# Performance work log

Hardware: AMD Instinct MI355X
Metric: run time of the kernel (lower is better)

The kernel has to match this reference:

```python
import jax, jax.numpy as jnp
import numpy as np
from jax import lax

BETA = 0.9   # membrane decay
THR = 1.0    # firing threshold (soft reset)
K = 10       # number of time bins
# spatial pyramid for original_shape=(100,368) under 4 stride-2 SAME convs
HW = [(50, 184), (25, 92), (13, 46), (7, 23)]
CH = [4, 8, 16, 32]


def conv(x, w, b, stride=1):
    y = lax.conv_general_dilated(x, w, (stride, stride), 'SAME',
                                 dimension_numbers=('NCHW', 'OIHW', 'NCHW'))
    return y + b[None, :, None, None]


def spike(u):
    # heaviside forward, sigmoid straight-through surrogate backward
    s = (u > 0.0).astype(u.dtype)
    sg = jax.nn.sigmoid(4.0 * u)
    return sg + lax.stop_gradient(s - sg)


def setup_inputs() -> dict:
    key = jax.random.key(0)
    ks = jax.random.split(key, 12)
    T, B = 1000, 1
    x = jax.random.normal(ks[0], (T, B, 1, 100, 368), jnp.float32)

    def w(k, o, i, kh=3, kw=3):
        return 0.1 * jax.random.normal(k, (o, i, kh, kw), jnp.float32)

    inp = {'x': x}
    cin = [1] + CH[:3]
    for li in range(4):
        inp['w%d' % (li + 1)] = w(ks[1 + li], CH[li], cin[li])
        inp['b%d' % (li + 1)] = jnp.zeros((CH[li],), jnp.float32)
    sc = [2 * K * c for c in CH]  # skip channels: [80,160,320,640]
    inp['dw4'] = w(ks[5], 64, sc[3]); inp['db4'] = jnp.zeros((64,), jnp.float32)
    inp['dw3'] = w(ks[6], 32, 64 + sc[2]); inp['db3'] = jnp.zeros((32,), jnp.float32)
    inp['dw2'] = w(ks[7], 16, 32 + sc[1]); inp['db2'] = jnp.zeros((16,), jnp.float32)
    inp['dw1'] = w(ks[8], 8, 16 + sc[0]); inp['db1'] = jnp.zeros((8,), jnp.float32)
    inp['wo'] = w(ks[9], 1, 8, 1, 1); inp['bo'] = jnp.zeros((1,), jnp.float32)
    inp['total_steps'] = 1000
    inp['block_size'] = 100
    return inp


def reference(x, w1, b1, w2, b2, w3, b3, w4, b4,
              dw4, db4, dw3, db3, dw2, db2, dw1, db1, wo, bo,
              total_steps, block_size):
    S = total_steps // K  # steps per bin
    B = x.shape[1]
    xb = x.reshape((K, S) + x.shape[1:])  # [K,S,B,C,H,W]
    mems0 = tuple(jnp.zeros((B, CH[i], HW[i][0], HW[i][1]), x.dtype) for i in range(4))
    enc_w = [(w1, b1), (w2, b2), (w3, b3), (w4, b4)]

    def forward_step(x_t, mems):
        new_mems, spk = [], x_t
        for (wi, bi), m in zip(enc_w, mems):
            m = BETA * m + conv(spk, wi, bi, 2)
            spk = spike(m - THR)
            m = m - spk * THR  # soft reset
            new_mems.append(m)
        return tuple(new_mems)

    def step(carry, x_t):
        mems, sums, sqs = carry
        mems = forward_step(x_t, mems)
        sums = tuple(s + m for s, m in zip(sums, mems))
        sqs = tuple(q + m * m for q, m in zip(sqs, mems))
        return (mems, sums, sqs), None

    def bin_fn(mems, x_bin):
        zeros = tuple(jnp.zeros_like(m) for m in mems)
        (mems, sums, sqs), _ = lax.scan(step, (mems, zeros, zeros), x_bin)
        means = tuple(s / S for s in sums)
        stds = tuple(jnp.sqrt(jnp.maximum(q / S - mu * mu, 1e-8))
                     for q, mu in zip(sqs, means))
        return mems, (means, stds)

    _, (means, stds) = lax.scan(bin_fn, mems0, xb)  # each leaf: [K,B,C,H,W]

    def skip(mean, std):
        # torch.cat([mean0,std0,mean1,std1,...], dim=1) channel ordering
        f = jnp.stack([mean, std], axis=1)        # [K,2,B,C,H,W]
        f = jnp.transpose(f, (2, 0, 1, 3, 4, 5))  # [B,K,2,C,H,W]
        b_, k_, t_, c_, h_, w_ = f.shape
        return f.reshape(b_, k_ * t_ * c_, h_, w_)

    skips = [skip(means[i], stds[i]) for i in range(4)]

    def up(t, hw):
        return jax.image.resize(t, (t.shape[0], t.shape[1], hw[0], hw[1]), 'bilinear')

    relu = jax.nn.relu
    d = relu(conv(skips[3], dw4, db4))
    d = relu(conv(jnp.concatenate([up(d, HW[2]), skips[2]], 1), dw3, db3))
    d = relu(conv(jnp.concatenate([up(d, HW[1]), skips[1]], 1), dw2, db2))
    d = relu(conv(jnp.concatenate([up(d, HW[0]), skips[0]], 1), dw1, db1))
    tau_c = conv(up(d, (100, 368)), wo, bo)  # [B,1,100,368]
    return tau_c
```

## Files before the change

kernel.cpp:

```cpp
#include <hip/hip_runtime.h>

#define KBINS  10
#define SBIN   100
#define BETA   0.9f
#define THR    1.0f
#define CDIV(a,b) (((a)+(b)-1)/(b))


__global__ void k_zero16(float4* __restrict__ p, int n16) {
    int i = blockIdx.x * blockDim.x + threadIdx.x;
    if (i < n16) p[i] = make_float4(0.f, 0.f, 0.f, 0.f);
}

__global__ void k_conv1(const float* __restrict__ x,
                        const float* __restrict__ w1,
                        const float* __restrict__ b1,
                        float* __restrict__ c1, int tcount) {
    int n = blockIdx.x * blockDim.x + threadIdx.x;
    if (n >= tcount * 50 * 46) return;
    int wq  = n % 46;
    int tmp = n / 46;
    int h   = tmp % 50;
    int t   = tmp / 50;
    int w0  = wq * 4;

    const float* xt = x + (size_t)t * 36800;
    float rm2 = (h  < 49)  ? 1.f : 0.f;
    float cm8 = (w0 < 180) ? 1.f : 0.f;
    int   r2  = min(2 * h + 2, 99);
    int   cb  = 2 * w0;
    int   c8  = min(cb + 8, 367);

    const float* row0 = xt + (2 * h) * 368 + cb;
    const float* row1 = row0 + 368;
    const float* row2 = xt + r2 * 368 + cb;

    float tap[3][9];
    #pragma unroll
    for (int j = 0; j < 8; j++) {
        tap[0][j] = row0[j];
        tap[1][j] = row1[j];
        tap[2][j] = row2[j] * rm2;
    }
    tap[0][8] = xt[(2 * h) * 368 + c8] * cm8;
    tap[1][8] = xt[(2 * h + 1) * 368 + c8] * cm8;
    tap[2][8] = xt[r2 * 368 + c8] * (rm2 * cm8);

    float* ot = c1 + (size_t)t * 36800 + h * 184 + w0;
    #pragma unroll
    for (int co = 0; co < 4; co++) {
        float b = b1[co];
        float a0 = b, a1 = b, a2 = b, a3 = b;
        #pragma unroll
        for (int r = 0; r < 3; r++) {
            #pragma unroll
            for (int kw = 0; kw < 3; kw++) {
                float wv = w1[co * 9 + r * 3 + kw];
                a0 = fmaf(tap[r][0 + kw], wv, a0);
                a1 = fmaf(tap[r][2 + kw], wv, a1);
                a2 = fmaf(tap[r][4 + kw], wv, a2);
                a3 = fmaf(tap[r][6 + kw], wv, a3);
            }
        }
        *(float4*)(ot + (size_t)co * 9200) = make_float4(a0, a1, a2, a3);
    }
}

__global__ void k_scan(const float* __restrict__ cbuf,
                       unsigned char* __restrict__ spk,
                       float* __restrict__ skip,
                       float* __restrict__ mstate,
                       int C, int HW, int Win, int Wp, int HpWp,
                       int write_spk, int bin0, int nbins, int init) {
    const int PF = 10;
    int CHW = C * HW;
    int p = blockIdx.x * blockDim.x + threadIdx.x;
    if (p >= CHW) return;
    int c  = p / HW;
    int hw = p - c * HW;
    int h  = hw / Win, w = hw - h * Win;

    const size_t tstr = (size_t)C * HpWp;
    unsigned char* sp = spk + (size_t)bin0 * SBIN * tstr
                      + (size_t)c * HpWp + (h + 1) * Wp + (w + 1);

    float m = init ? 0.0f : mstate[p];
    float va[PF], vb[PF];
    #pragma unroll
    for (int j = 0; j < PF; j++) va[j] = cbuf[(size_t)j * CHW + p];

    int T = nbins * SBIN;
    for (int k = 0; k < nbins; k++) {
        float s = 0.0f, q = 0.0f;
        for (int b = 0; b < SBIN / PF; b++) {
            int lt0 = k * SBIN + b * PF;
            int ltn = lt0 + PF;
            bool more = (ltn < T);
            #pragma unroll
            for (int j = 0; j < PF; j++)
                vb[j] = more ? cbuf[(size_t)(ltn + j) * CHW + p] : 0.0f;
            #pragma unroll
            for (int j = 0; j < PF; j++) {
                m = fmaf(m, BETA, va[j]);
                float spv = (m - THR > 0.0f) ? 1.0f : 0.0f;
                m -= spv * THR;
                if (write_spk) sp[(size_t)(lt0 + j) * tstr] = (unsigned char)spv;
                s += m;
                q = fmaf(m, m, q);
            }
            #pragma unroll
            for (int j = 0; j < PF; j++) va[j] = vb[j];
        }
        int g = bin0 + k;
        float mean = s * (1.0f / SBIN);
        float var  = q * (1.0f / SBIN) - mean * mean;
        float sd   = sqrtf(fmaxf(var, 1e-8f));
        skip[(size_t)(g * 2 * C + c) * HW + hw]     = mean;
        skip[(size_t)(g * 2 * C + C + c) * HW + hw] = sd;
    }
    mstate[p] = m;
}

template<int CIN, int COUT, int COG, int OW,
         int HOUT, int WOUT, int PADH, int HP, int WP>
__global__ void k_convs2(const unsigned char* __restrict__ spk,
                         const float* __restrict__ wt,
                         const float* __restrict__ bias,
                         float* __restrict__ out, int t0, int tcount) {
    const int WQ = (WOUT + OW - 1) / OW;
    const int NT = 2 * OW + 1;
    int n = blockIdx.x * blockDim.x + threadIdx.x;
    if (n >= tcount * HOUT * WQ) return;
    int wq  = n % WQ;
    int tmp = n / WQ;
    int h   = tmp % HOUT;
    int tl  = tmp / HOUT;
    int cog = blockIdx.y;
    int w0  = wq * OW;

    const unsigned char* base = spk + (size_t)(t0 + tl) * CIN * HP * WP
                              + (2 * h - PADH + 1) * WP + (2 * w0 + 1);

    float acc[OW][COG];
    #pragma unroll
    for (int q = 0; q < OW; q++)
        #pragma unroll
        for (int co = 0; co < COG; co++) acc[q][co] = bias[cog * COG + co];

    for (int ci = 0; ci < CIN; ci++) {
        const unsigned char* ic = base + (size_t)ci * HP * WP;
        float tap[3][NT];
        #pragma unroll
        for (int r = 0; r < 3; r++)
            #pragma unroll
            for (int j = 0; j < NT; j++)
                tap[r][j] = (float)ic[r * WP + j];
        #pragma unroll
        for (int co = 0; co < COG; co++) {
            const float* wc = wt + ((size_t)(cog * COG + co) * CIN + ci) * 9;
            #pragma unroll
            for (int r = 0; r < 3; r++)
                #pragma unroll
                for (int kw = 0; kw < 3; kw++) {
                    float wv = wc[r * 3 + kw];
                    #pragma unroll
                    for (int q = 0; q < OW; q++)
                        acc[q][co] = fmaf(tap[r][2 * q + kw], wv, acc[q][co]);
                }
        }
    }

    float* ot = out + ((size_t)tl * COUT + cog * COG) * (HOUT * WOUT) + h * WOUT + w0;
    #pragma unroll
    for (int co = 0; co < COG; co++) {
        float* oc = ot + (size_t)co * (HOUT * WOUT);
        if constexpr (OW == 4) {
            *(float4*)oc = make_float4(acc[0][co], acc[1][co], acc[2][co], acc[3][co]);
        } else {
            if (w0 + 2 <= WOUT) *(float2*)oc = make_float2(acc[0][co], acc[1][co]);
            else                oc[0] = acc[0][co];
        }
    }
}

__global__ void k_conv_part(const float* __restrict__ in, int Cin, int H, int W,
                            const float* __restrict__ wt,
                            float* __restrict__ part,
                            int Cout, int CS) {
    int HW  = H * W;
    int pix = blockIdx.x * blockDim.x + threadIdx.x;
    if (pix >= HW) return;
    int co    = blockIdx.y;
    int chunk = blockIdx.z;
    int h = pix / W, w = pix - h * W;

    int off[9]; float msk[9];
    #pragma unroll
    for (int kh = 0; kh < 3; kh++) {
        int r = h + kh - 1;
        bool rok = (r >= 0) && (r < H);
        int rc = rok ? r : 0;
        #pragma unroll
        for (int kw = 0; kw < 3; kw++) {
            int cc = w + kw - 1;
            bool cok = (cc >= 0) && (cc < W);
            int ccc = cok ? cc : 0;
            off[kh * 3 + kw] = rc * W + ccc;
            msk[kh * 3 + kw] = (rok && cok) ? 1.0f : 0.0f;
        }
    }

    const float* ibase = in + (size_t)chunk * CS * HW;
    const float* wbase = wt + ((size_t)co * Cin + (size_t)chunk * CS) * 9;
    float acc0 = 0.0f, acc1 = 0.0f;
    for (int ci = 0; ci < CS; ci += 2) {
        const float* ic0 = ibase + (size_t)ci * HW;
        const float* wc0 = wbase + ci * 9;
        #pragma unroll
        for (int j = 0; j < 9; j++)
            acc0 = fmaf(msk[j] * ic0[off[j]], wc0[j], acc0);
        const float* ic1 = ic0 + HW;
        const float* wc1 = wc0 + 9;
        #pragma unroll
        for (int j = 0; j < 9; j++)
            acc1 = fmaf(msk[j] * ic1[off[j]], wc1[j], acc1);
    }
    part[((size_t)chunk * Cout + co) * HW + pix] = acc0 + acc1;
}

__global__ void k_dconv_part(const float* __restrict__ skp, int Cskip,
                             const float* __restrict__ dprev, int Cup,
                             int Hi, int Wi,
                             const float* __restrict__ wt,
                             float* __restrict__ part,
                             int Cout, int CS, int H, int W) {
    int HW  = H * W;
    int pix = blockIdx.x * blockDim.x + threadIdx.x;
    if (pix >= HW) return;
    int co    = blockIdx.y;
    int chunk = blockIdx.z;
    int h = pix / W, w = pix - h * W;
    int Cin = Cup + Cskip;

    int roff[3], h0c[3], h1c[3];
    float rmsk[3], ah[3];
    #pragma unroll
    for (int kh = 0; kh < 3; kh++) {
        int r = h + kh - 1;
        bool rok = (r >= 0) && (r < H);
        roff[kh] = rok ? r : 0;
        rmsk[kh] = rok ? 1.0f : 0.0f;
        float ph = (r + 0.5f) * (float)Hi / (float)H - 0.5f;
        float fh = floorf(ph);
        ah[kh] = ph - fh;
        int hh = (int)fh;
        h0c[kh] = min(max(hh, 0), Hi - 1);
        h1c[kh] = min(max(hh + 1, 0), Hi - 1);
    }
    int coff[3], w0c[3], w1c[3];
    float cmsk[3], aw[3];
    #pragma unroll
    for (int kw = 0; kw < 3; kw++) {
        int cc = w + kw - 1;
        bool cok = (cc >= 0) && (cc < W);
        coff[kw] = cok ? cc : 0;
        cmsk[kw] = cok ? 1.0f : 0.0f;
        float pw = (cc + 0.5f) * (float)Wi / (float)W - 0.5f;
        float fw = floorf(pw);
        aw[kw] = pw - fw;
        int ww = (int)fw;
        w0c[kw] = min(max(ww, 0), Wi - 1);
        w1c[kw] = min(max(ww + 1, 0), Wi - 1);
    }

    float acc0 = 0.0f, acc1 = 0.0f;
    for (int cl = 0; cl < CS; cl++) {
        int ci = chunk * CS + cl;
        const float* wc = wt + ((size_t)co * Cin + ci) * 9;
        float a = 0.0f;
        if (ci < Cup) {
            const float* dc = dprev + (size_t)ci * Hi * Wi;
            #pragma unroll
            for (int kh = 0; kh < 3; kh++) {
                #pragma unroll
                for (int kw = 0; kw < 3; kw++) {
                    float v00 = dc[h0c[kh] * Wi + w0c[kw]];
                    float v01 = dc[h0c[kh] * Wi + w1c[kw]];
                    float v10 = dc[h1c[kh] * Wi + w0c[kw]];
                    float v11 = dc[h1c[kh] * Wi + w1c[kw]];
                    float v = (1.0f - ah[kh]) * ((1.0f - aw[kw]) * v00 + aw[kw] * v01)
                            + ah[kh] * ((1.0f - aw[kw]) * v10 + aw[kw] * v11);
                    a = fmaf(v * rmsk[kh] * cmsk[kw], wc[kh * 3 + kw], a);
                }
            }
        } else {
            const float* ic = skp + (size_t)(ci - Cup) * HW;
            #pragma unroll
            for (int kh = 0; kh < 3; kh++)
                #pragma unroll
                for (int kw = 0; kw < 3; kw++)
                    a = fmaf(rmsk[kh] * cmsk[kw] * ic[roff[kh] * W + coff[kw]],
                             wc[kh * 3 + kw], a);
        }
        if (cl & 1) acc1 += a; else acc0 += a;
    }
    part[((size_t)chunk * Cout + co) * HW + pix] = acc0 + acc1;
}

__global__ void k_reduce_relu(const float* __restrict__ part,
                              const float* __restrict__ bias,
                              float* __restrict__ out,
                              int Cout, int HW, int nchunks) {
    int n = blockIdx.x * blockDim.x + threadIdx.x;
    if (n >= Cout * HW) return;
    int co = n / HW;
    float acc = bias[co];
    for (int c = 0; c < nchunks; c++)
        acc += part[(size_t)c * Cout * HW + n];
    out[n] = fmaxf(acc, 0.0f);
}

__global__ void k_final(const float* __restrict__ d1,
                        const float* __restrict__ wo,
                        const float* __restrict__ bo,
                        float* __restrict__ out) {
    int n = blockIdx.x * blockDim.x + threadIdx.x;
    if (n >= 36800) return;
    int w = n % 368, h = n / 368;
    float ph = (h + 0.5f) * 0.5f - 0.5f;
    float pw = (w + 0.5f) * 0.5f - 0.5f;
    float fh = floorf(ph), fw = floorf(pw);
    int h0 = (int)fh, w0 = (int)fw;
    float ah = ph - fh, aw = pw - fw;
    int h0c = min(max(h0, 0), 49),  h1c = min(max(h0 + 1, 0), 49);
    int w0c = min(max(w0, 0), 183), w1c = min(max(w0 + 1, 0), 183);
    float acc = bo[0];
    #pragma unroll
    for (int c = 0; c < 8; c++) {
        const float* sc = d1 + c * 9200;
        float v00 = sc[h0c * 184 + w0c], v01 = sc[h0c * 184 + w1c];
        float v10 = sc[h1c * 184 + w0c], v11 = sc[h1c * 184 + w1c];
        float v = (1.0f - ah) * ((1.0f - aw) * v00 + aw * v01)
                + ah * ((1.0f - aw) * v10 + aw * v11);
        acc = fmaf(wo[c], v, acc);
    }
    out[n] = acc;
}

extern "C" void kernel_launch(void* const* d_in, const int* in_sizes, int n_in,
                              void* d_out, int out_size, void* d_ws, size_t ws_size,
                              hipStream_t stream) {
    (void)in_sizes; (void)n_in; (void)out_size; (void)ws_size;
    const float* x   = (const float*)d_in[0];
    const float* w1  = (const float*)d_in[1];
    const float* b1  = (const float*)d_in[2];
    const float* w2  = (const float*)d_in[3];
    const float* b2  = (const float*)d_in[4];
    const float* w3  = (const float*)d_in[5];
    const float* b3  = (const float*)d_in[6];
    const float* w4  = (const float*)d_in[7];
    const float* b4  = (const float*)d_in[8];
    const float* dw4 = (const float*)d_in[9];
    const float* db4 = (const float*)d_in[10];
    const float* dw3 = (const float*)d_in[11];
    const float* db3 = (const float*)d_in[12];
    const float* dw2 = (const float*)d_in[13];
    const float* db2 = (const float*)d_in[14];
    const float* dw1 = (const float*)d_in[15];
    const float* db1 = (const float*)d_in[16];
    const float* wo  = (const float*)d_in[17];
    const float* bo  = (const float*)d_in[18];
    float* out = (float*)d_out;

    char* ws = (char*)d_ws;
    size_t off = 0;
    auto alloc = [&](size_t bytes) -> void* {
        void* p = ws + off;
        off += (bytes + 255) & ~(size_t)255;
        return p;
    };
    float*         cbuf  = (float*)alloc(38272000);
    unsigned char* spk1p = (unsigned char*)alloc(39936000);
    unsigned char* spk2p = (unsigned char*)alloc(21600000);
    unsigned char* spk3p = (unsigned char*)alloc(12960000);
    float*         skip0 = (float*)alloc(2944000);
    float*         skip1 = (float*)alloc(1472000);
    float*         skip2 = (float*)alloc(765440);
    float*         skip3 = (float*)alloc(412160);
    float*         ms1   = (float*)alloc(147200);
    float*         ms2   = (float*)alloc(73600);
    char* dec = (char*)cbuf;
    size_t doff = 0;
    auto dalloc = [&](size_t bytes) -> void* {
        void* p = dec + doff;
        doff += (bytes + 255) & ~(size_t)255;
        return p;
    };
    float* d4   = (float*)dalloc(10304u * 4);
    float* d3   = (float*)dalloc(19136u * 4);
    float* d2   = (float*)dalloc(36800u * 4);
    float* d1   = (float*)dalloc(73600u * 4);
    float* part = (float*)dalloc(2500000u);

    const int BS  = 256;
    const int SBS = 64;

    {
        int n16 = (39936000 + 21600000 + 12960000) / 16;
        k_zero16<<<CDIV(n16, BS), BS, 0, stream>>>((float4*)spk1p, n16);
    }

    for (int q = 0; q < 5; q++) {
        k_conv1<<<CDIV(200 * 50 * 46, BS), BS, 0, stream>>>(
            x + (size_t)q * 200 * 36800, w1, b1, cbuf, 200);
        k_scan<<<CDIV(36800, SBS), SBS, 0, stream>>>(
            cbuf, spk1p, skip0, ms1, 4, 9200, 184, 192, 52 * 192,
            1, 2 * q, 2, (q == 0) ? 1 : 0);
    }

    for (int q = 0; q < 2; q++) {
        k_convs2<4, 8, 8, 4, 25, 92, 0, 52, 192>
            <<<dim3(CDIV(500 * 25 * 23, BS), 1), BS, 0, stream>>>(
                spk1p, w2, b2, cbuf, q * 500, 500);
        k_scan<<<CDIV(18400, SBS), SBS, 0, stream>>>(
            cbuf, spk2p, skip1, ms2, 8, 2300, 92, 100, 27 * 100,
            1, 5 * q, 5, (q == 0) ? 1 : 0);
    }

    k_convs2<8, 16, 16, 2, 13, 46, 1, 27, 100>
        <<<dim3(CDIV(1000 * 13 * 23, BS), 1), BS, 0, stream>>>(
            spk2p, w3, b3, cbuf, 0, 1000);
    k_scan<<<CDIV(9568, SBS), SBS, 0, stream>>>(
        cbuf, spk3p, skip2, ms2, 16, 598, 46, 54, 15 * 54, 1, 0, 10, 1);

    k_convs2<16, 32, 16, 2, 7, 23, 1, 15, 54>
        <<<dim3(CDIV(1000 * 7 * 12, BS), 2), BS, 0, stream>>>(
            spk3p, w4, b4, cbuf, 0, 1000);
    k_scan<<<CDIV(5152, SBS), SBS, 0, stream>>>(
        cbuf, spk3p , skip3, ms1 , 32, 161, 23, 31, 9 * 31,
        0, 0, 10, 1);

    {
        dim3 g(CDIV(161, 64), 64, 10);
        k_conv_part<<<g, 64, 0, stream>>>(skip3, 640, 7, 23, dw4, part, 64, 64);
        k_reduce_relu<<<CDIV(64 * 161, BS), BS, 0, stream>>>(part, db4, d4, 64, 161, 10);
    }
    {
        dim3 g(CDIV(598, 64), 32, 8);
        k_dconv_part<<<g, 64, 0, stream>>>(skip2, 320, d4, 64, 7, 23,
                                           dw3, part, 32, 48, 13, 46);
        k_reduce_relu<<<CDIV(32 * 598, BS), BS, 0, stream>>>(part, db3, d3, 32, 598, 8);
    }
    {
        dim3 g(CDIV(2300, BS), 16, 4);
        k_dconv_part<<<g, BS, 0, stream>>>(skip1, 160, d3, 32, 13, 46,
                                           dw2, part, 16, 48, 25, 92);
        k_reduce_relu<<<CDIV(16 * 2300, BS), BS, 0, stream>>>(part, db2, d2, 16, 2300, 4);
    }
    {
        dim3 g(CDIV(9200, BS), 8, 2);
        k_dconv_part<<<g, BS, 0, stream>>>(skip0, 80, d2, 16, 25, 92,
                                           dw1, part, 8, 48, 50, 184);
        k_reduce_relu<<<CDIV(8 * 9200, BS), BS, 0, stream>>>(part, db1, d1, 8, 9200, 2);
    }
    k_final<<<CDIV(36800, BS), BS, 0, stream>>>(d1, wo, bo, out);
}
```

Measured before the change: 968.2 us.

## Run encoder layers over all timesteps at once and fuse decoder reduction via atomics

The time-chunked loops for layers 1 and 2 are replaced by single full-length conv and scan launches, using a much larger conv buffer that holds all 1000 timesteps. This removes the per-chunk membrane state carry and several launches. The decoder's partial-sum buffers and separate reduce+ReLU kernels are replaced by atomicAdd into zeroed outputs, with ReLU moved into the consumers' loads. The scan prefetch depth is raised to 20. In exchange, working-set memory and cache pressure grow, and the atomics make the decoder sums order-dependent.

```diff
diff --git a/kernel.cpp b/kernel.cpp
--- a/kernel.cpp
+++ b/kernel.cpp
@@ -15,9 +15,9 @@
 __global__ void k_conv1(const float* __restrict__ x,
                         const float* __restrict__ w1,
                         const float* __restrict__ b1,
-                        float* __restrict__ c1, int tcount) {
+                        float* __restrict__ c1) {
     int n = blockIdx.x * blockDim.x + threadIdx.x;
-    if (n >= tcount * 50 * 46) return;
+    if (n >= 1000 * 50 * 46) return;
     int wq  = n % 46;
     int tmp = n / 46;
     int h   = tmp % 50;
@@ -69,10 +69,9 @@
 __global__ void k_scan(const float* __restrict__ cbuf,
                        unsigned char* __restrict__ spk,
                        float* __restrict__ skip,
-                       float* __restrict__ mstate,
-                       int C, int HW, int Win, int Wp, int HpWp,
-                       int write_spk, int bin0, int nbins, int init) {
-    const int PF = 10;
+                       float* __restrict__ mscratch,
+                       int C, int HW, int Win, int Wp, int HpWp, int write_spk) {
+    const int PF = 20;
     int CHW = C * HW;
     int p = blockIdx.x * blockDim.x + threadIdx.x;
     if (p >= CHW) return;
@@ -81,44 +80,42 @@
     int h  = hw / Win, w = hw - h * Win;
 
     const size_t tstr = (size_t)C * HpWp;
-    unsigned char* sp = spk + (size_t)bin0 * SBIN * tstr
-                      + (size_t)c * HpWp + (h + 1) * Wp + (w + 1);
-
-    float m = init ? 0.0f : mstate[p];
+    unsigned char* sp = spk + (size_t)c * HpWp + (h + 1) * Wp + (w + 1);
+
+    float m = 0.0f;
     float va[PF], vb[PF];
     #pragma unroll
     for (int j = 0; j < PF; j++) va[j] = cbuf[(size_t)j * CHW + p];
 
-    int T = nbins * SBIN;
-    for (int k = 0; k < nbins; k++) {
+    const int T = KBINS * SBIN;
+    for (int k = 0; k < KBINS; k++) {
         float s = 0.0f, q = 0.0f;
         for (int b = 0; b < SBIN / PF; b++) {
-            int lt0 = k * SBIN + b * PF;
-            int ltn = lt0 + PF;
-            bool more = (ltn < T);
+            int t0 = k * SBIN + b * PF;
+            int tn = t0 + PF;
+            bool more = (tn < T);
             #pragma unroll
             for (int j = 0; j < PF; j++)
-                vb[j] = more ? cbuf[(size_t)(ltn + j) * CHW + p] : 0.0f;
+                vb[j] = more ? cbuf[(size_t)(tn + j) * CHW + p] : 0.0f;
             #pragma unroll
             for (int j = 0; j < PF; j++) {
                 m = fmaf(m, BETA, va[j]);
                 float spv = (m - THR > 0.0f) ? 1.0f : 0.0f;
                 m -= spv * THR;
-                if (write_spk) sp[(size_t)(lt0 + j) * tstr] = (unsigned char)spv;
+                if (write_spk) sp[(size_t)(t0 + j) * tstr] = (unsigned char)spv;
                 s += m;
                 q = fmaf(m, m, q);
             }
             #pragma unroll
             for (int j = 0; j < PF; j++) va[j] = vb[j];
         }
-        int g = bin0 + k;
         float mean = s * (1.0f / SBIN);
         float var  = q * (1.0f / SBIN) - mean * mean;
         float sd   = sqrtf(fmaxf(var, 1e-8f));
-        skip[(size_t)(g * 2 * C + c) * HW + hw]     = mean;
-        skip[(size_t)(g * 2 * C + C + c) * HW + hw] = sd;
-    }
-    mstate[p] = m;
+        skip[(size_t)(k * 2 * C + c) * HW + hw]     = mean;
+        skip[(size_t)(k * 2 * C + C + c) * HW + hw] = sd;
+    }
+    mscratch[p] = m;
 }
 
 template<int CIN, int COUT, int COG, int OW,
@@ -126,19 +123,19 @@
 __global__ void k_convs2(const unsigned char* __restrict__ spk,
                          const float* __restrict__ wt,
                          const float* __restrict__ bias,
-                         float* __restrict__ out, int t0, int tcount) {
+                         float* __restrict__ out) {
     const int WQ = (WOUT + OW - 1) / OW;
     const int NT = 2 * OW + 1;
     int n = blockIdx.x * blockDim.x + threadIdx.x;
-    if (n >= tcount * HOUT * WQ) return;
+    if (n >= 1000 * HOUT * WQ) return;
     int wq  = n % WQ;
     int tmp = n / WQ;
     int h   = tmp % HOUT;
-    int tl  = tmp / HOUT;
+    int t   = tmp / HOUT;
     int cog = blockIdx.y;
     int w0  = wq * OW;
 
-    const unsigned char* base = spk + (size_t)(t0 + tl) * CIN * HP * WP
+    const unsigned char* base = spk + (size_t)t * CIN * HP * WP
                               + (2 * h - PADH + 1) * WP + (2 * w0 + 1);
 
     float acc[OW][COG];
@@ -170,7 +167,7 @@
         }
     }
 
-    float* ot = out + ((size_t)tl * COUT + cog * COG) * (HOUT * WOUT) + h * WOUT + w0;
+    float* ot = out + ((size_t)t * COUT + cog * COG) * (HOUT * WOUT) + h * WOUT + w0;
     #pragma unroll
     for (int co = 0; co < COG; co++) {
         float* oc = ot + (size_t)co * (HOUT * WOUT);
@@ -183,9 +180,10 @@
     }
 }
 
-__global__ void k_conv_part(const float* __restrict__ in, int Cin, int H, int W,
+__global__ void k_dec_conv0(const float* __restrict__ in, int Cin, int H, int W,
                             const float* __restrict__ wt,
-                            float* __restrict__ part,
+                            const float* __restrict__ bias,
+                            float* __restrict__ dout,
                             int Cout, int CS) {
     int HW  = H * W;
     int pix = blockIdx.x * blockDim.x + threadIdx.x;
@@ -212,7 +210,8 @@
 
     const float* ibase = in + (size_t)chunk * CS * HW;
     const float* wbase = wt + ((size_t)co * Cin + (size_t)chunk * CS) * 9;
-    float acc0 = 0.0f, acc1 = 0.0f;
+    float acc0 = (chunk == 0) ? bias[co] : 0.0f;
+    float acc1 = 0.0f;
     for (int ci = 0; ci < CS; ci += 2) {
         const float* ic0 = ibase + (size_t)ci * HW;
         const float* wc0 = wbase + ci * 9;
@@ -225,15 +224,16 @@
         for (int j = 0; j < 9; j++)
             acc1 = fmaf(msk[j] * ic1[off[j]], wc1[j], acc1);
     }
-    part[((size_t)chunk * Cout + co) * HW + pix] = acc0 + acc1;
-}
-
-__global__ void k_dconv_part(const float* __restrict__ skp, int Cskip,
-                             const float* __restrict__ dprev, int Cup,
-                             int Hi, int Wi,
-                             const float* __restrict__ wt,
-                             float* __restrict__ part,
-                             int Cout, int CS, int H, int W) {
+    atomicAdd(&dout[(size_t)co * HW + pix], acc0 + acc1);
+}
+
+__global__ void k_dec_conv(const float* __restrict__ skp, int Cskip,
+                           const float* __restrict__ dprev, int Cup,
+                           int Hi, int Wi,
+                           const float* __restrict__ wt,
+                           const float* __restrict__ bias,
+                           float* __restrict__ dout,
+                           int Cout, int CS, int H, int W) {
     int HW  = H * W;
     int pix = blockIdx.x * blockDim.x + threadIdx.x;
     if (pix >= HW) return;
@@ -273,7 +273,8 @@
         w1c[kw] = min(max(ww + 1, 0), Wi - 1);
     }
 
-    float acc0 = 0.0f, acc1 = 0.0f;
+    float acc0 = (chunk == 0) ? bias[co] : 0.0f;
+    float acc1 = 0.0f;
     for (int cl = 0; cl < CS; cl++) {
         int ci = chunk * CS + cl;
         const float* wc = wt + ((size_t)co * Cin + ci) * 9;
@@ -284,10 +285,10 @@
             for (int kh = 0; kh < 3; kh++) {
                 #pragma unroll
                 for (int kw = 0; kw < 3; kw++) {
-                    float v00 = dc[h0c[kh] * Wi + w0c[kw]];
-                    float v01 = dc[h0c[kh] * Wi + w1c[kw]];
-                    float v10 = dc[h1c[kh] * Wi + w0c[kw]];
-                    float v11 = dc[h1c[kh] * Wi + w1c[kw]];
+                    float v00 = fmaxf(dc[h0c[kh] * Wi + w0c[kw]], 0.0f);
+                    float v01 = fmaxf(dc[h0c[kh] * Wi + w1c[kw]], 0.0f);
+                    float v10 = fmaxf(dc[h1c[kh] * Wi + w0c[kw]], 0.0f);
+                    float v11 = fmaxf(dc[h1c[kh] * Wi + w1c[kw]], 0.0f);
                     float v = (1.0f - ah[kh]) * ((1.0f - aw[kw]) * v00 + aw[kw] * v01)
                             + ah[kh] * ((1.0f - aw[kw]) * v10 + aw[kw] * v11);
                     a = fmaf(v * rmsk[kh] * cmsk[kw], wc[kh * 3 + kw], a);
@@ -304,20 +305,7 @@
         }
         if (cl & 1) acc1 += a; else acc0 += a;
     }
-    part[((size_t)chunk * Cout + co) * HW + pix] = acc0 + acc1;
-}
-
-__global__ void k_reduce_relu(const float* __restrict__ part,
-                              const float* __restrict__ bias,
-                              float* __restrict__ out,
-                              int Cout, int HW, int nchunks) {
-    int n = blockIdx.x * blockDim.x + threadIdx.x;
-    if (n >= Cout * HW) return;
-    int co = n / HW;
-    float acc = bias[co];
-    for (int c = 0; c < nchunks; c++)
-        acc += part[(size_t)c * Cout * HW + n];
-    out[n] = fmaxf(acc, 0.0f);
+    atomicAdd(&dout[(size_t)co * HW + pix], acc0 + acc1);
 }
 
 __global__ void k_final(const float* __restrict__ d1,
@@ -338,8 +326,10 @@
     #pragma unroll
     for (int c = 0; c < 8; c++) {
         const float* sc = d1 + c * 9200;
-        float v00 = sc[h0c * 184 + w0c], v01 = sc[h0c * 184 + w1c];
-        float v10 = sc[h1c * 184 + w0c], v11 = sc[h1c * 184 + w1c];
+        float v00 = fmaxf(sc[h0c * 184 + w0c], 0.0f);
+        float v01 = fmaxf(sc[h0c * 184 + w1c], 0.0f);
+        float v10 = fmaxf(sc[h1c * 184 + w0c], 0.0f);
+        float v11 = fmaxf(sc[h1c * 184 + w1c], 0.0f);
         float v = (1.0f - ah) * ((1.0f - aw) * v00 + aw * v01)
                 + ah * ((1.0f - aw) * v10 + aw * v11);
         acc = fmaf(wo[c], v, acc);
@@ -379,89 +369,67 @@
         off += (bytes + 255) & ~(size_t)255;
         return p;
     };
-    float*         cbuf  = (float*)alloc(38272000);
+    float*         cbuf  = (float*)alloc(147200000);
     unsigned char* spk1p = (unsigned char*)alloc(39936000);
     unsigned char* spk2p = (unsigned char*)alloc(21600000);
     unsigned char* spk3p = (unsigned char*)alloc(12960000);
+    float*         d4    = (float*)alloc(41216);
+    float*         d3    = (float*)alloc(76544);
+    float*         d2    = (float*)alloc(147200);
+    float*         d1    = (float*)alloc(294400);
     float*         skip0 = (float*)alloc(2944000);
     float*         skip1 = (float*)alloc(1472000);
     float*         skip2 = (float*)alloc(765440);
     float*         skip3 = (float*)alloc(412160);
-    float*         ms1   = (float*)alloc(147200);
-    float*         ms2   = (float*)alloc(73600);
-    char* dec = (char*)cbuf;
-    size_t doff = 0;
-    auto dalloc = [&](size_t bytes) -> void* {
-        void* p = dec + doff;
-        doff += (bytes + 255) & ~(size_t)255;
-        return p;
-    };
-    float* d4   = (float*)dalloc(10304u * 4);
-    float* d3   = (float*)dalloc(19136u * 4);
-    float* d2   = (float*)dalloc(36800u * 4);
-    float* d1   = (float*)dalloc(73600u * 4);
-    float* part = (float*)dalloc(2500000u);
+    float*         msS   = (float*)alloc(147200);
 
     const int BS  = 256;
     const int SBS = 64;
 
     {
-        int n16 = (39936000 + 21600000 + 12960000) / 16;
+        size_t nb = 39936000ull + 21600000 + 12960000
+                  + 41216 + 76544 + 147200 + 294400;
+        int n16 = (int)(nb / 16);
         k_zero16<<<CDIV(n16, BS), BS, 0, stream>>>((float4*)spk1p, n16);
     }
 
-    for (int q = 0; q < 5; q++) {
-        k_conv1<<<CDIV(200 * 50 * 46, BS), BS, 0, stream>>>(
-            x + (size_t)q * 200 * 36800, w1, b1, cbuf, 200);
-        k_scan<<<CDIV(36800, SBS), SBS, 0, stream>>>(
-            cbuf, spk1p, skip0, ms1, 4, 9200, 184, 192, 52 * 192,
-            1, 2 * q, 2, (q == 0) ? 1 : 0);
-    }
-
-    for (int q = 0; q < 2; q++) {
-        k_convs2<4, 8, 8, 4, 25, 92, 0, 52, 192>
-            <<<dim3(CDIV(500 * 25 * 23, BS), 1), BS, 0, stream>>>(
-                spk1p, w2, b2, cbuf, q * 500, 500);
-        k_scan<<<CDIV(18400, SBS), SBS, 0, stream>>>(
-            cbuf, spk2p, skip1, ms2, 8, 2300, 92, 100, 27 * 100,
-            1, 5 * q, 5, (q == 0) ? 1 : 0);
-    }
+    k_conv1<<<CDIV(1000 * 50 * 46, BS), BS, 0, stream>>>(x, w1, b1, cbuf);
+    k_scan<<<CDIV(36800, SBS), SBS, 0, stream>>>(cbuf, spk1p, skip0, msS,
+                                                 4, 9200, 184, 192, 52 * 192, 1);
+
+    k_convs2<4, 8, 8, 4, 25, 92, 0, 52, 192>
+        <<<dim3(CDIV(1000 * 25 * 23, BS), 1), BS, 0, stream>>>(spk1p, w2, b2, cbuf);
+    k_scan<<<CDIV(18400, SBS), SBS, 0, stream>>>(cbuf, spk2p, skip1, msS,
+                                                 8, 2300, 92, 100, 27 * 100, 1);
 
     k_convs2<8, 16, 16, 2, 13, 46, 1, 27, 100>
-        <<<dim3(CDIV(1000 * 13 * 23, BS), 1), BS, 0, stream>>>(
-            spk2p, w3, b3, cbuf, 0, 1000);
-    k_scan<<<CDIV(9568, SBS), SBS, 0, stream>>>(
-        cbuf, spk3p, skip2, ms2, 16, 598, 46, 54, 15 * 54, 1, 0, 10, 1);
+        <<<dim3(CDIV(1000 * 13 * 23, BS), 1), BS, 0, stream>>>(spk2p, w3, b3, cbuf);
+    k_scan<<<CDIV(9568, SBS), SBS, 0, stream>>>(cbuf, spk3p, skip2, msS,
+                                                16, 598, 46, 54, 15 * 54, 1);
 
     k_convs2<16, 32, 16, 2, 7, 23, 1, 15, 54>
-        <<<dim3(CDIV(1000 * 7 * 12, BS), 2), BS, 0, stream>>>(
-            spk3p, w4, b4, cbuf, 0, 1000);
-    k_scan<<<CDIV(5152, SBS), SBS, 0, stream>>>(
-        cbuf, spk3p , skip3, ms1 , 32, 161, 23, 31, 9 * 31,
-        0, 0, 10, 1);
+        <<<dim3(CDIV(1000 * 7 * 12, BS), 2), BS, 0, stream>>>(spk3p, w4, b4, cbuf);
+    k_scan<<<CDIV(5152, SBS), SBS, 0, stream>>>(cbuf, spk1p , skip3, msS,
+                                                32, 161, 23, 31, 9 * 31, 0);
 
     {
         dim3 g(CDIV(161, 64), 64, 10);
-        k_conv_part<<<g, 64, 0, stream>>>(skip3, 640, 7, 23, dw4, part, 64, 64);
-        k_reduce_relu<<<CDIV(64 * 161, BS), BS, 0, stream>>>(part, db4, d4, 64, 161, 10);
+        k_dec_conv0<<<g, 64, 0, stream>>>(skip3, 640, 7, 23, dw4, db4, d4, 64, 64);
     }
     {
         dim3 g(CDIV(598, 64), 32, 8);
-        k_dconv_part<<<g, 64, 0, stream>>>(skip2, 320, d4, 64, 7, 23,
-                                           dw3, part, 32, 48, 13, 46);
-        k_reduce_relu<<<CDIV(32 * 598, BS), BS, 0, stream>>>(part, db3, d3, 32, 598, 8);
+        k_dec_conv<<<g, 64, 0, stream>>>(skip2, 320, d4, 64, 7, 23,
+                                         dw3, db3, d3, 32, 48, 13, 46);
     }
     {
-        dim3 g(CDIV(2300, BS), 16, 4);
-        k_dconv_part<<<g, BS, 0, stream>>>(skip1, 160, d3, 32, 13, 46,
-                                           dw2, part, 16, 48, 25, 92);
-        k_reduce_relu<<<CDIV(16 * 2300, BS), BS, 0, stream>>>(part, db2, d2, 16, 2300, 4);
+        dim3 g(CDIV(2300, 128), 16, 4);
+        k_dec_conv<<<g, 128, 0, stream>>>(skip1, 160, d3, 32, 13, 46,
+                                          dw2, db2, d2, 16, 48, 25, 92);
     }
     {
         dim3 g(CDIV(9200, BS), 8, 2);
-        k_dconv_part<<<g, BS, 0, stream>>>(skip0, 80, d2, 16, 25, 92,
-                                           dw1, part, 8, 48, 50, 184);
-        k_reduce_relu<<<CDIV(8 * 9200, BS), BS, 0, stream>>>(part, db1, d1, 8, 9200, 2);
+        k_dec_conv<<<g, BS, 0, stream>>>(skip0, 80, d2, 16, 25, 92,
+                                         dw1, db1, d1, 8, 48, 50, 184);
     }
     k_final<<<CDIV(36800, BS), BS, 0, stream>>>(d1, wo, bo, out);
 }
```

New measurement: 1.061 ms. +9.5%, slower.
